# Kernel optimization log

Hardware: AMD Instinct MI355X
Metric: run time of the kernel (lower is better)

The kernel has to match this reference:

```python
import jax, jax.numpy as jnp
import numpy as np

B, N, D = 4, 2048, 512      # batch, seq, dim_in
DK = DV = 512               # dim_k == dim_v (required by fc input width)
NH = 8
HK = DK // NH               # per-head dk == dv == 64
SCALE = 1.0 / np.sqrt(HK)
LN_EPS = 1e-5


def setup_inputs() -> dict:
    key = jax.random.key(0)
    ks = jax.random.split(key, 8)
    s = 0.02
    return {
        "x": jax.random.normal(ks[0], (B, N, D), dtype=jnp.float32),
        "Wq": jax.random.normal(ks[1], (D, DK), dtype=jnp.float32) * s,
        "Wk": jax.random.normal(ks[2], (D, DK), dtype=jnp.float32) * s,
        "Wv": jax.random.normal(ks[3], (D, DV), dtype=jnp.float32) * s,
        "Wf": jax.random.normal(ks[4], (2 * DK, D), dtype=jnp.float32) * s,
        "bf": jnp.zeros((D,), dtype=jnp.float32),
        "gamma": jnp.ones((D,), dtype=jnp.float32),
        "beta": jnp.zeros((D,), dtype=jnp.float32),
    }


def reference(x, Wq, Wk, Wv, Wf, bf, gamma, beta):
    b, n, _ = x.shape
    # projections -> [b, nh, n, hk]; q_c/q_f etc. are identical in the source,
    # so compute once.
    def proj(W):
        return jnp.einsum('bnd,dk->bnk', x, W).reshape(b, n, NH, -1).transpose(0, 2, 1, 3)
    q, k, v = proj(Wq), proj(Wk), proj(Wv)

    # conventional branch: softmax over n x n scores
    dist_c = jax.nn.softmax(jnp.einsum('bhqd,bhkd->bhqk', q, k) * SCALE, axis=-1)
    att_c = jnp.einsum('bhqk,bhkd->bhqd', dist_c, v)          # [b,nh,n,hk]
    att_c = att_c.transpose(0, 2, 1, 3).reshape(b, n, DV)

    # feature branch: softmax over dk x dk scores (linear-complexity variant)
    dist_f = jax.nn.softmax(jnp.einsum('bhnk,bhnq->bhkq', k, q) * SCALE, axis=-1)
    att_f = jnp.einsum('bhnd,bhdq->bhnq', v, dist_f)           # [b,nh,n,hk]
    att_f = att_f.transpose(0, 2, 1, 3).reshape(b, n, DV)

    att = jnp.concatenate([att_c, att_f], axis=2)              # [b,n,2*dk]
    out = jax.nn.relu(att @ Wf + bf)                           # dropout=eval (identity)
    out = out + x
    mu = jnp.mean(out, axis=-1, keepdims=True)
    var = jnp.var(out, axis=-1, keepdims=True)
    out = (out - mu) * jax.lax.rsqrt(var + LN_EPS) * gamma + beta
    return out
```

## Files before the change

### kernel.cpp

```cpp
#include <hip/hip_runtime.h>
#include <math.h>
#include <stdint.h>

#define B_   4
#define N_   2048
#define D_   512
#define DK_  512
#define NH_  8
#define HK_  64
#define LN_EPS_ 1e-5f
#define QS_  0.18033688011112042f

typedef unsigned short u16;
typedef __attribute__((ext_vector_type(8))) short short8;
typedef __attribute__((ext_vector_type(4))) float f32x4;
typedef __attribute__((ext_vector_type(8))) unsigned short u16x8;

__device__ __forceinline__ u16 f2bf(float x) {
    uint32_t u = __builtin_bit_cast(uint32_t, x);
    return (u16)((u + 0x7fffu + ((u >> 16) & 1u)) >> 16);
}
__device__ __forceinline__ u16 f2bf_fast(float x) {
    return (u16)((__builtin_bit_cast(uint32_t, x) + 0x8000u) >> 16);
}
__device__ __forceinline__ float b2f(u16 v) {
    return __builtin_bit_cast(float, (uint32_t)v << 16);
}
__device__ __forceinline__ uint32_t cvtpk_bf16(float lo, float hi) {
    uint32_t r;
    asm("v_cvt_pk_bf16_f32 %0, %1, %2" : "=v"(r) : "v"(lo), "v"(hi));
    return r;
}
__device__ __forceinline__ float exp2f_fast(float x) {
    return __builtin_amdgcn_exp2f(x);
}

__device__ __forceinline__ void gload16(const void* g, void* l) {
    __builtin_amdgcn_global_load_lds(
        reinterpret_cast<const __attribute__((address_space(1))) void*>(
            reinterpret_cast<uintptr_t>(g)),
        reinterpret_cast<__attribute__((address_space(3))) void*>(
            static_cast<uint32_t>(reinterpret_cast<uintptr_t>(l))),
        16, 0, 0);
}

__global__ __launch_bounds__(256) void prep_kernel(
    const float* __restrict__ x, const float* __restrict__ Wq,
    const float* __restrict__ Wk, const float* __restrict__ Wv,
    const float* __restrict__ Wf, u16* __restrict__ xb,
    u16* __restrict__ wqkvT, u16* __restrict__ wfT)
{
    __shared__ float t[32][33];
    const int bid = blockIdx.x, tid = threadIdx.x;
    if (bid < 2048) {
        const int i = (bid * 256 + tid) * 8;
        const float4 a = *reinterpret_cast<const float4*>(&x[i]);
        const float4 b = *reinterpret_cast<const float4*>(&x[i + 4]);
        u16x8 o;
        o[0] = f2bf(a.x); o[1] = f2bf(a.y); o[2] = f2bf(a.z); o[3] = f2bf(a.w);
        o[4] = f2bf(b.x); o[5] = f2bf(b.y); o[6] = f2bf(b.z); o[7] = f2bf(b.w);
        *reinterpret_cast<u16x8*>(&xb[i]) = o;
        return;
    }
    const float* W;
    u16* dst;
    int K, Nc, nt, kt;
    if (bid < 2816) {
        const int z = (bid - 2048) >> 8, rem = (bid - 2048) & 255;
        W = z == 0 ? Wq : (z == 1 ? Wk : Wv);
        dst = wqkvT + (size_t)z * 512 * 512;
        K = 512; Nc = 512;
        nt = (rem & 15) * 32; kt = (rem >> 4) * 32;
    } else {
        const int rem = bid - 2816;
        W = Wf; dst = wfT; K = 1024; Nc = 512;
        nt = (rem & 15) * 32; kt = (rem >> 4) * 32;
    }
    {
        const int r = tid >> 3, c0 = (tid & 7) * 4;
        const float4 v = *reinterpret_cast<const float4*>(
            &W[(size_t)(kt + r) * Nc + nt + c0]);
        t[r][c0] = v.x; t[r][c0 + 1] = v.y; t[r][c0 + 2] = v.z; t[r][c0 + 3] = v.w;
    }
    __syncthreads();
    {
        const int nidx = tid >> 3, kc = (tid & 7) * 4;
        u16 o[4];
        #pragma unroll
        for (int j = 0; j < 4; ++j) o[j] = f2bf(t[kc + j][nidx]);
        *reinterpret_cast<ushort4*>(&dst[(size_t)(nt + nidx) * K + kt + kc]) =
            make_ushort4(o[0], o[1], o[2], o[3]);
    }
}

template<int BM, int BN, int MODE>
__global__ __launch_bounds__(256) void gemm_bf16(
    const u16* __restrict__ A, const u16* __restrict__ Bt,
    u16* __restrict__ qb, u16* __restrict__ kb,
    u16* __restrict__ vb, u16* __restrict__ vt, int M, int Nc, int K,
    const float* __restrict__ bias, const float* __restrict__ resid)
{
    constexpr int MI = BM / 32, NI = BN / 32;
    constexpr int AL = BM / 32, BL = BN / 32;
    __shared__ u16 As[BM * 64];
    __shared__ u16 Bs[BN * 64];
    const int tid = threadIdx.x;
    const int lane = tid & 63, wave = tid >> 6;
    const int wm = wave >> 1, wn = wave & 1;
    const int l15 = lane & 15, lg = lane >> 4;

    const int nwg = gridDim.x;
    const int bid = ((int)blockIdx.x & 7) * (nwg >> 3) + ((int)blockIdx.x >> 3);
    const int ntiles = Nc / BN;
    const int nt = (bid % ntiles) * BN;
    const int mt = (bid / ntiles) * BM;

    f32x4 acc[MI][NI] = {};

    for (int kt = 0; kt < K; kt += 64) {
        __syncthreads();
        #pragma unroll
        for (int i = 0; i < AL; ++i) {
            const int ob = (wave * AL + i) * 1024;
            const int o = ob + lane * 16;
            const int row = o >> 7;
            const int inner = (o & 127) ^ ((row & 7) << 4);
            gload16((const char*)A + ((size_t)(mt + row) * K + kt) * 2 + inner,
                    (char*)As + ob);
        }
        #pragma unroll
        for (int i = 0; i < BL; ++i) {
            const int ob = (wave * BL + i) * 1024;
            const int o = ob + lane * 16;
            const int row = o >> 7;
            const int inner = (o & 127) ^ ((row & 7) << 4);
            gload16((const char*)Bt + ((size_t)(nt + row) * K + kt) * 2 + inner,
                    (char*)Bs + ob);
        }
        __syncthreads();
        #pragma unroll
        for (int ks = 0; ks < 2; ++ks) {
            const int kb2 = ks * 32 + lg * 8;
            short8 af[MI], bfr[NI];
            #pragma unroll
            for (int mi = 0; mi < MI; ++mi) {
                const int r = wm * (BM / 2) + mi * 16 + l15;
                af[mi] = *reinterpret_cast<const short8*>(
                    &As[r * 64 + (kb2 ^ ((r & 7) << 3))]);
            }
            #pragma unroll
            for (int ni = 0; ni < NI; ++ni) {
                const int r = wn * (BN / 2) + ni * 16 + l15;
                bfr[ni] = *reinterpret_cast<const short8*>(
                    &Bs[r * 64 + (kb2 ^ ((r & 7) << 3))]);
            }
            #pragma unroll
            for (int mi = 0; mi < MI; ++mi)
                #pragma unroll
                for (int ni = 0; ni < NI; ++ni)
                    acc[mi][ni] = __builtin_amdgcn_mfma_f32_16x16x32_bf16(
                        af[mi], bfr[ni], acc[mi][ni], 0, 0, 0);
        }
    }

    #pragma unroll
    for (int mi = 0; mi < MI; ++mi) {
        #pragma unroll
        for (int ni = 0; ni < NI; ++ni) {
            const int col = nt + wn * (BN / 2) + ni * 16 + l15;
            const int row0 = mt + wm * (BM / 2) + mi * 16 + lg * 4;
            if (MODE == 1) {
                if (col < 512) {
                    #pragma unroll
                    for (int jj = 0; jj < 4; ++jj)
                        qb[(size_t)(row0 + jj) * 512 + col] =
                            f2bf(acc[mi][ni][jj] * QS_);
                } else if (col < 1024) {
                    #pragma unroll
                    for (int jj = 0; jj < 4; ++jj)
                        kb[(size_t)(row0 + jj) * 512 + col - 512] =
                            f2bf(acc[mi][ni][jj]);
                } else {
                    const int dfull = col - 1024;
                    const int hh = dfull >> 6, dd = dfull & 63;
                    const int bb = row0 >> 11, nn = row0 & 2047;
                    u16 o4[4];
                    #pragma unroll
                    for (int jj = 0; jj < 4; ++jj) {
                        o4[jj] = f2bf(acc[mi][ni][jj]);
                        vb[(size_t)(row0 + jj) * 512 + dfull] = o4[jj];
                    }
                    *reinterpret_cast<ushort4*>(
                        &vt[(((size_t)(bb * NH_ + hh)) * HK_ + dd) * N_ + nn]) =
                        make_ushort4(o4[0], o4[1], o4[2], o4[3]);
                }
            } else {
                #pragma unroll
                for (int jj = 0; jj < 4; ++jj) {
                    const size_t row = (size_t)(row0 + jj);
                    float v = acc[mi][ni][jj];
                    v += bias[col];
                    v = fmaxf(v, 0.0f);
                    v += resid[row * Nc + col];
                    qb[row * Nc + col] = f2bf(v);
                }
            }
        }
    }
}

__global__ __launch_bounds__(256) void flash_featS_kernel(
    const u16* __restrict__ Qb, const u16* __restrict__ Kb,
    const u16* __restrict__ Vt, u16* __restrict__ att,
    float* __restrict__ partials)
{
    __shared__ u16 sh[24576];
    const int tid = threadIdx.x;
    const int lane = tid & 63, wave = tid >> 6;
    const int l15 = lane & 15, lg = lane >> 4;

    if ((int)blockIdx.x >= 512) {
        u16* KsT = sh;
        u16* QsT = sh + 4096;
        const int fid = (int)blockIdx.x - 512;
        const int ns = fid & 7, h = (fid >> 3) & 7, b = fid >> 6;
        const size_t hbase = (size_t)b * N_ * DK_ + (size_t)h * HK_;

        f32x4 acc[4] = {};
        for (int c = 0; c < 4; ++c) {
            const int n0 = ns * 256 + c * 64;
            __syncthreads();
            #pragma unroll
            for (int it = 0; it < 2; ++it) {
                const int idx = tid + it * 256;
                const int n = idx >> 3, d0 = (idx & 7) * 8;
                const u16x8 kv = *reinterpret_cast<const u16x8*>(
                    &Kb[hbase + (size_t)(n0 + n) * DK_ + d0]);
                const u16x8 qv = *reinterpret_cast<const u16x8*>(
                    &Qb[hbase + (size_t)(n0 + n) * DK_ + d0]);
                #pragma unroll
                for (int j = 0; j < 8; ++j) {
                    const int r = d0 + j;
                    const int cidx = n ^ ((r & 7) << 3);
                    KsT[r * 64 + cidx] = kv[j];
                    QsT[r * 64 + cidx] = qv[j];
                }
            }
            __syncthreads();
            #pragma unroll
            for (int ks = 0; ks < 2; ++ks) {
                const int kb2 = ks * 32 + lg * 8;
                const int ar = wave * 16 + l15;
                const short8 aK = *reinterpret_cast<const short8*>(
                    &KsT[ar * 64 + (kb2 ^ ((ar & 7) << 3))]);
                #pragma unroll
                for (int ni = 0; ni < 4; ++ni) {
                    const int br = ni * 16 + l15;
                    const short8 bQ = *reinterpret_cast<const short8*>(
                        &QsT[br * 64 + (kb2 ^ ((br & 7) << 3))]);
                    acc[ni] = __builtin_amdgcn_mfma_f32_16x16x32_bf16(
                        aK, bQ, acc[ni], 0, 0, 0);
                }
            }
        }
        const int bh = b * NH_ + h;
        #pragma unroll
        for (int ni = 0; ni < 4; ++ni)
            #pragma unroll
            for (int jj = 0; jj < 4; ++jj) {
                const int row = wave * 16 + lg * 4 + jj;
                partials[(((size_t)ns * 32 + bh) * 64 + row) * 64 + ni * 16 + l15] =
                    acc[ni][jj];
            }
        return;
    }

    u16* kb0 = sh;
    u16* kb1 = sh + 4096;
    u16* vb0 = sh + 8192;
    u16* vb1 = sh + 12288;
    u16* Ps  = sh + 16384;
    const int lbid = (((int)blockIdx.x & 7) << 6) + ((int)blockIdx.x >> 3);
    const int qt = lbid & 15, h = (lbid >> 4) & 7, b = lbid >> 7;

    short8 aq[2][2];
    #pragma unroll
    for (int qs = 0; qs < 2; ++qs) {
        const int qrow = qt * 128 + qs * 64 + wave * 16 + l15;
        const u16* qp = Qb + ((size_t)(b * N_ + qrow)) * DK_ + h * HK_ + lg * 8;
        aq[qs][0] = *reinterpret_cast<const short8*>(qp);
        aq[qs][1] = *reinterpret_cast<const short8*>(qp + 32);
    }
    short8 ones;
    #pragma unroll
    for (int i = 0; i < 8; ++i) ones[i] = (short)0x3F80;

    const u16* Kbase = Kb + (size_t)b * N_ * DK_ + (size_t)h * HK_;
    const u16* Vbase = Vt + ((size_t)(b * NH_ + h)) * HK_ * N_;
    unsigned long long* Ps64 = reinterpret_cast<unsigned long long*>(Ps);

    f32x4 o[2][5] = {};
    float m_[2] = {-1e30f, -1e30f};
    f32x4 SA[2][4], SB[2][4];

    const int ob0 = wave * 1024, oo0 = ob0 + lane * 16;
    const int row0s = oo0 >> 7;
    const int in0 = (oo0 & 127) ^ ((row0s & 7) << 4);

#define STAGE_K(ktile, KBUF) do {                                              \
    gload16((const char*)Kbase +                                               \
                ((size_t)((ktile) * 64 + row0s) * DK_) * 2 + in0,              \
            (char*)(KBUF) + ob0);                                              \
    gload16((const char*)Kbase +                                               \
                ((size_t)((ktile) * 64 + 32 + row0s) * DK_) * 2 + in0,         \
            (char*)(KBUF) + 4096 + ob0);                                       \
} while (0)

#define STAGE_V(ktile, VBUF) do {                                              \
    gload16((const char*)Vbase +                                               \
                ((size_t)row0s * N_ + (ktile) * 64) * 2 + in0,                 \
            (char*)(VBUF) + ob0);                                              \
    gload16((const char*)Vbase +                                               \
                ((size_t)(32 + row0s) * N_ + (ktile) * 64) * 2 + in0,          \
            (char*)(VBUF) + 4096 + ob0);                                       \
} while (0)

#define QK_STEP(S, KBUF) do {                                                  \
    _Pragma("unroll")                                                          \
    for (int qs = 0; qs < 2; ++qs)                                             \
        _Pragma("unroll")                                                      \
        for (int t = 0; t < 4; ++t)                                            \
            S[qs][t] = (f32x4){0.0f, 0.0f, 0.0f, 0.0f};                        \
    __builtin_amdgcn_s_setprio(1);                                             \
    _Pragma("unroll")                                                          \
    for (int ks = 0; ks < 2; ++ks) {                                           \
        const int kb2 = ks * 32 + lg * 8;                                      \
        _Pragma("unroll")                                                      \
        for (int t = 0; t < 4; ++t) {                                          \
            const int r = t * 16 + l15;                                        \
            const short8 bk = *reinterpret_cast<const short8*>(                \
                &(KBUF)[r * 64 + (kb2 ^ ((r & 7) << 3))]);                     \
            S[0][t] = __builtin_amdgcn_mfma_f32_16x16x32_bf16(                 \
                bk, aq[0][ks], S[0][t], 0, 0, 0);                              \
            S[1][t] = __builtin_amdgcn_mfma_f32_16x16x32_bf16(                 \
                bk, aq[1][ks], S[1][t], 0, 0, 0);                              \
        }                                                                      \
    }                                                                          \
    __builtin_amdgcn_s_setprio(0);                                             \
} while (0)

#define SMPV_STEP(S, VBUF) do {                                                \
    float rmax[2], cm;                                                         \
    _Pragma("unroll")                                                          \
    for (int qs = 0; qs < 2; ++qs) {                                           \
        float a0 = fmaxf(fmaxf(S[qs][0][0], S[qs][0][1]),                      \
                         fmaxf(S[qs][0][2], S[qs][0][3]));                     \
        float a1 = fmaxf(fmaxf(S[qs][1][0], S[qs][1][1]),                      \
                         fmaxf(S[qs][1][2], S[qs][1][3]));                     \
        float a2 = fmaxf(fmaxf(S[qs][2][0], S[qs][2][1]),                      \
                         fmaxf(S[qs][2][2], S[qs][2][3]));                     \
        float a3 = fmaxf(fmaxf(S[qs][3][0], S[qs][3][1]),                      \
                         fmaxf(S[qs][3][2], S[qs][3][3]));                     \
        rmax[qs] = fmaxf(fmaxf(a0, a1), fmaxf(a2, a3));                        \
    }                                                                          \
    cm = fmaxf(rmax[0] - m_[0], rmax[1] - m_[1]);                              \
    if (__any(cm > 8.0f)) {                                                    \
        _Pragma("unroll")                                                      \
        for (int qs = 0; qs < 2; ++qs) {                                       \
            float rm = rmax[qs];                                               \
            rm = fmaxf(rm, __shfl_xor(rm, 16));                                \
            rm = fmaxf(rm, __shfl_xor(rm, 32));                                \
            const float newm = fmaxf(m_[qs], rm);                              \
            const float fac = exp2f_fast(m_[qs] - newm);                       \
            m_[qs] = newm;                                                     \
            float facq[4];                                                     \
            _Pragma("unroll")                                                  \
            for (int jj = 0; jj < 4; ++jj)                                     \
                facq[jj] = __shfl(fac, lg * 4 + jj);                           \
            _Pragma("unroll")                                                  \
            for (int t = 0; t < 5; ++t)                                        \
                _Pragma("unroll")                                              \
                for (int jj = 0; jj < 4; ++jj)                                 \
                    o[qs][t][jj] *= facq[jj];                                  \
        }                                                                      \
    }                                                                          \
    _Pragma("unroll")                                                          \
    for (int qs = 0; qs < 2; ++qs) {                                           \
        const int prow = qs * 64 + wave * 16 + l15;                            \
        const int pb64 = prow * 16;                                            \
        const int sw1 = (prow & 7) << 1;                                       \
        _Pragma("unroll")                                                      \
        for (int t = 0; t < 4; ++t) {                                          \
            const float p0 = exp2f_fast(S[qs][t][0] - m_[qs]);                 \
            const float p1 = exp2f_fast(S[qs][t][1] - m_[qs]);                 \
            const float p2 = exp2f_fast(S[qs][t][2] - m_[qs]);                 \
            const float p3 = exp2f_fast(S[qs][t][3] - m_[qs]);                 \
            const uint32_t lo = cvtpk_bf16(p0, p1);                            \
            const uint32_t hi = cvtpk_bf16(p2, p3);                            \
            Ps64[pb64 + ((t * 4 + lg) ^ sw1)] =                                \
                (unsigned long long)lo | ((unsigned long long)hi << 32);       \
        }                                                                      \
    }                                                                          \
    __builtin_amdgcn_s_setprio(1);                                             \
    _Pragma("unroll")                                                          \
    for (int ks = 0; ks < 2; ++ks) {                                           \
        const int kb2 = ks * 32 + lg * 8;                                      \
        const int pr0 = wave * 16 + l15;                                       \
        const int pr1 = 64 + pr0;                                              \
        const short8 ap0 = *reinterpret_cast<const short8*>(                   \
            &Ps[pr0 * 64 + (kb2 ^ ((pr0 & 7) << 3))]);                         \
        const short8 ap1 = *reinterpret_cast<const short8*>(                   \
            &Ps[pr1 * 64 + (kb2 ^ ((pr1 & 7) << 3))]);                         \
        _Pragma("unroll")                                                      \
        for (int t = 0; t < 4; ++t) {                                          \
            const int dr = t * 16 + l15;                                       \
            const short8 bv = *reinterpret_cast<const short8*>(                \
                &(VBUF)[dr * 64 + (kb2 ^ ((dr & 7) << 3))]);                   \
            o[0][t] = __builtin_amdgcn_mfma_f32_16x16x32_bf16(                 \
                ap0, bv, o[0][t], 0, 0, 0);                                    \
            o[1][t] = __builtin_amdgcn_mfma_f32_16x16x32_bf16(                 \
                ap1, bv, o[1][t], 0, 0, 0);                                    \
        }                                                                      \
        o[0][4] = __builtin_amdgcn_mfma_f32_16x16x32_bf16(                     \
            ap0, ones, o[0][4], 0, 0, 0);                                      \
        o[1][4] = __builtin_amdgcn_mfma_f32_16x16x32_bf16(                     \
            ap1, ones, o[1][4], 0, 0, 0);                                      \
    }                                                                          \
    __builtin_amdgcn_s_setprio(0);                                             \
} while (0)

    STAGE_K(0, kb0);
    STAGE_K(1, kb1);
    STAGE_V(0, vb0);
    __syncthreads();
    QK_STEP(SA, kb0);

    #pragma unroll 1
    for (int t2 = 0; t2 < 30; t2 += 2) {
        __syncthreads();
        STAGE_K(t2 + 2, kb0);
        STAGE_V(t2 + 1, vb1);
        QK_STEP(SB, kb1);
        SMPV_STEP(SA, vb0);
        __syncthreads();
        STAGE_K(t2 + 3, kb1);
        STAGE_V(t2 + 2, vb0);
        QK_STEP(SA, kb0);
        SMPV_STEP(SB, vb1);
    }
    __syncthreads();
    STAGE_V(31, vb1);
    QK_STEP(SB, kb1);
    SMPV_STEP(SA, vb0);
    __syncthreads();
    SMPV_STEP(SB, vb1);

#undef STAGE_K
#undef STAGE_V
#undef QK_STEP
#undef SMPV_STEP

    #pragma unroll
    for (int qs = 0; qs < 2; ++qs)
        #pragma unroll
        for (int jj = 0; jj < 4; ++jj) {
            const float inv = 1.0f / o[qs][4][jj];
            const size_t row = (size_t)b * N_ + qt * 128 + qs * 64 + wave * 16 + lg * 4 + jj;
            #pragma unroll
            for (int t = 0; t < 4; ++t)
                att[row * (2 * DK_) + h * HK_ + t * 16 + l15] =
                    f2bf_fast(o[qs][t][jj] * inv);
        }
}

__global__ __launch_bounds__(256) void featSM_kernel(
    const float* __restrict__ partials, u16* __restrict__ distfT)
{
    const int bh = blockIdx.x, tid = threadIdx.x;
    const int r = tid >> 2, qq = tid & 3;
    float v[16];
    #pragma unroll
    for (int j = 0; j < 16; ++j) v[j] = 0.0f;
    for (int s = 0; s < 8; ++s) {
        const float4* pp = reinterpret_cast<const float4*>(
            &partials[(((size_t)s * 32 + bh) * 64 + r) * 64 + qq * 16]);
        #pragma unroll
        for (int j4 = 0; j4 < 4; ++j4) {
            const float4 a = pp[j4];
            v[j4 * 4 + 0] += a.x; v[j4 * 4 + 1] += a.y;
            v[j4 * 4 + 2] += a.z; v[j4 * 4 + 3] += a.w;
        }
    }
    float m = v[0];
    #pragma unroll
    for (int j = 1; j < 16; ++j) m = fmaxf(m, v[j]);
    m = fmaxf(m, __shfl_xor(m, 1));
    m = fmaxf(m, __shfl_xor(m, 2));
    float sum = 0.0f;
    #pragma unroll
    for (int j = 0; j < 16; ++j) { v[j] = exp2f_fast(v[j] - m); sum += v[j]; }
    sum += __shfl_xor(sum, 1);
    sum += __shfl_xor(sum, 2);
    const float inv = 1.0f / sum;
    #pragma unroll
    for (int j = 0; j < 16; ++j)
        distfT[(size_t)bh * 4096 + (qq * 16 + j) * 64 + r] = f2bf_fast(v[j] * inv);
}

__global__ __launch_bounds__(256) void featAV_mfma(
    const u16* __restrict__ V, const u16* __restrict__ distfT,
    u16* __restrict__ att)
{
    __shared__ u16 Bs[64 * 64];
    __shared__ u16 As[64 * 64];
    const int tid = threadIdx.x;
    const int lane = tid & 63, wave = tid >> 6;
    const int l15 = lane & 15, lg = lane >> 4;
    const int ns = blockIdx.x, h = blockIdx.y, b = blockIdx.z;
    const int bh = b * NH_ + h;

    #pragma unroll
    for (int it = 0; it < 2; ++it) {
        const int idx = tid + it * 256;
        const int r = idx >> 3, c0 = (idx & 7) * 8;
        const u16x8 dv = *reinterpret_cast<const u16x8*>(
            &distfT[(size_t)bh * 4096 + r * 64 + c0]);
        *reinterpret_cast<u16x8*>(&Bs[r * 64 + (c0 ^ ((r & 7) << 3))]) = dv;
    }

    for (int c = 0; c < 4; ++c) {
        const int n0 = ns * 256 + c * 64;
        __syncthreads();
        #pragma unroll
        for (int i = 0; i < 2; ++i) {
            const int ob = (wave * 2 + i) * 1024;
            const int o_ = ob + lane * 16;
            const int row = o_ >> 7;
            const int inner = (o_ & 127) ^ ((row & 7) << 4);
            gload16((const char*)V + ((size_t)(b * N_ + n0 + row) * DK_ + h * HK_) * 2 + inner,
                    (char*)As + ob);
        }
        __syncthreads();
        f32x4 acc[4] = {};
        #pragma unroll
        for (int ks = 0; ks < 2; ++ks) {
            const int kb2 = ks * 32 + lg * 8;
            const int ar = wave * 16 + l15;
            const short8 av = *reinterpret_cast<const short8*>(
                &As[ar * 64 + (kb2 ^ ((ar & 7) << 3))]);
            #pragma unroll
            for (int ni = 0; ni < 4; ++ni) {
                const int br = ni * 16 + l15;
                const short8 bd = *reinterpret_cast<const short8*>(
                    &Bs[br * 64 + (kb2 ^ ((br & 7) << 3))]);
                acc[ni] = __builtin_amdgcn_mfma_f32_16x16x32_bf16(av, bd, acc[ni], 0, 0, 0);
            }
        }
        #pragma unroll
        for (int ni = 0; ni < 4; ++ni)
            #pragma unroll
            for (int jj = 0; jj < 4; ++jj)
                att[((size_t)b * N_ + n0 + wave * 16 + lg * 4 + jj) * (2 * DK_)
                    + 512 + h * HK_ + ni * 16 + l15] = f2bf_fast(acc[ni][jj]);
    }
}

__global__ __launch_bounds__(256) void ln_kernel(
    const u16* __restrict__ fc, const float* __restrict__ gamma,
    const float* __restrict__ beta, float* __restrict__ out)
{
    const int row = blockIdx.x * 4 + (threadIdx.x >> 6);
    const int lane = threadIdx.x & 63;
    const int c = lane * 8;
    const u16x8 v = *reinterpret_cast<const u16x8*>(&fc[(size_t)row * D_ + c]);
    float f[8];
    float s = 0.0f, sq = 0.0f;
    #pragma unroll
    for (int j = 0; j < 8; ++j) {
        f[j] = b2f(v[j]);
        s += f[j];
        sq = fmaf(f[j], f[j], sq);
    }
    #pragma unroll
    for (int off = 32; off >= 1; off >>= 1) {
        s  += __shfl_xor(s, off);
        sq += __shfl_xor(sq, off);
    }
    const float mu = s * (1.0f / D_);
    const float var = sq * (1.0f / D_) - mu * mu;
    const float rstd = rsqrtf(var + LN_EPS_);
    const float4 g0 = *reinterpret_cast<const float4*>(&gamma[c]);
    const float4 g1 = *reinterpret_cast<const float4*>(&gamma[c + 4]);
    const float4 b0 = *reinterpret_cast<const float4*>(&beta[c]);
    const float4 b1 = *reinterpret_cast<const float4*>(&beta[c + 4]);
    const float gg[8] = {g0.x, g0.y, g0.z, g0.w, g1.x, g1.y, g1.z, g1.w};
    const float bb[8] = {b0.x, b0.y, b0.z, b0.w, b1.x, b1.y, b1.z, b1.w};
    float4 o0, o1;
    o0.x = (f[0] - mu) * rstd * gg[0] + bb[0];
    o0.y = (f[1] - mu) * rstd * gg[1] + bb[1];
    o0.z = (f[2] - mu) * rstd * gg[2] + bb[2];
    o0.w = (f[3] - mu) * rstd * gg[3] + bb[3];
    o1.x = (f[4] - mu) * rstd * gg[4] + bb[4];
    o1.y = (f[5] - mu) * rstd * gg[5] + bb[5];
    o1.z = (f[6] - mu) * rstd * gg[6] + bb[6];
    o1.w = (f[7] - mu) * rstd * gg[7] + bb[7];
    *reinterpret_cast<float4*>(&out[(size_t)row * D_ + c]) = o0;
    *reinterpret_cast<float4*>(&out[(size_t)row * D_ + c + 4]) = o1;
}

extern "C" void kernel_launch(void* const* d_in, const int* in_sizes, int n_in,
                              void* d_out, int out_size, void* d_ws, size_t ws_size,
                              hipStream_t stream)
{
    (void)in_sizes; (void)n_in; (void)out_size; (void)ws_size;
    const float* x     = (const float*)d_in[0];
    const float* Wq    = (const float*)d_in[1];
    const float* Wk    = (const float*)d_in[2];
    const float* Wv    = (const float*)d_in[3];
    const float* Wf    = (const float*)d_in[4];
    const float* bf    = (const float*)d_in[5];
    const float* gamma = (const float*)d_in[6];
    const float* beta  = (const float*)d_in[7];
    float* out = (float*)d_out;

    char* w = (char*)d_ws;
    const size_t SZE = (size_t)B_ * N_ * DK_;
    u16* xb     = (u16*)w;   w += SZE * 2;
    u16* wqkvT  = (u16*)w;   w += (size_t)1536 * 512 * 2;
    u16* wfT    = (u16*)w;   w += (size_t)512 * 1024 * 2;
    u16* qb     = (u16*)w;   w += SZE * 2;
    u16* kb     = (u16*)w;   w += SZE * 2;
    u16* vb     = (u16*)w;   w += SZE * 2;
    u16* vt     = (u16*)w;   w += SZE * 2;
    u16* attb   = (u16*)w;   w += SZE * 2 * 2;
    float* partials = (float*)w; w += (size_t)8 * 32 * 4096 * 4;
    u16* distfT = (u16*)w;   w += (size_t)32 * 4096 * 2;
    u16* fcout  = (u16*)w;

    const dim3 blk(256);
    const int M = B_ * N_;

    prep_kernel<<<dim3(3328), blk, 0, stream>>>(x, Wq, Wk, Wv, Wf, xb, wqkvT, wfT);

    gemm_bf16<128, 128, 1><<<dim3(768), blk, 0, stream>>>(
        xb, wqkvT, qb, kb, vb, vt, M, 1536, 512, nullptr, nullptr);

    flash_featS_kernel<<<dim3(768), blk, 0, stream>>>(qb, kb, vt, attb, partials);

    featSM_kernel<<<dim3(32), blk, 0, stream>>>(partials, distfT);
    featAV_mfma<<<dim3(8, NH_, B_), blk, 0, stream>>>(vb, distfT, attb);

    gemm_bf16<64, 128, 2><<<dim3(512), blk, 0, stream>>>(
        attb, wfT, fcout, nullptr, nullptr, nullptr, M, D_, 2 * DK_, bf, x);

    ln_kernel<<<dim3(2048), blk, 0, stream>>>(fcout, gamma, beta, out);
}
```

Baseline: 126.2 us.

## Fuse feature-branch score, softmax and AV into flash kernel tail blocks

The feature-branch blocks inside the flash kernel now each own one (batch, head): they accumulate the full 64x64 K^T Q scores over all 2048 rows, apply the softmax in registers, stage the bf16 distribution in shared memory, and then compute V·dist for every row. This removes the separate partial-score buffer, the softmax kernel and the AV kernel along with their launches and global round trips. In exchange, only 32 feature blocks remain instead of 256, each running a long serial loop over 32 chunks twice, so the feature branch may become the tail of the flash launch.

```diff
diff --git a/kernel.cpp b/kernel.cpp
--- a/kernel.cpp
+++ b/kernel.cpp
@@ -209,10 +209,10 @@
     }
 }
 
-__global__ __launch_bounds__(256) void flash_featS_kernel(
+__global__ __launch_bounds__(256) void flash_feat_kernel(
     const u16* __restrict__ Qb, const u16* __restrict__ Kb,
-    const u16* __restrict__ Vt, u16* __restrict__ att,
-    float* __restrict__ partials)
+    const u16* __restrict__ Vt, const u16* __restrict__ Vb,
+    u16* __restrict__ att)
 {
     __shared__ u16 sh[24576];
     const int tid = threadIdx.x;
@@ -222,13 +222,15 @@
     if ((int)blockIdx.x >= 512) {
         u16* KsT = sh;
         u16* QsT = sh + 4096;
+        u16* BsD = sh + 8192;
+        u16* AsV = sh;
         const int fid = (int)blockIdx.x - 512;
-        const int ns = fid & 7, h = (fid >> 3) & 7, b = fid >> 6;
+        const int h = fid & 7, b = fid >> 3;
         const size_t hbase = (size_t)b * N_ * DK_ + (size_t)h * HK_;
 
         f32x4 acc[4] = {};
-        for (int c = 0; c < 4; ++c) {
-            const int n0 = ns * 256 + c * 64;
+        for (int c = 0; c < 32; ++c) {
+            const int n0 = c * 64;
             __syncthreads();
             #pragma unroll
             for (int it = 0; it < 2; ++it) {
@@ -263,15 +265,80 @@
                 }
             }
         }
-        const int bh = b * NH_ + h;
+
+        float dv[4][4];
         #pragma unroll
-        for (int ni = 0; ni < 4; ++ni)
-            #pragma unroll
-            for (int jj = 0; jj < 4; ++jj) {
-                const int row = wave * 16 + lg * 4 + jj;
-                partials[(((size_t)ns * 32 + bh) * 64 + row) * 64 + ni * 16 + l15] =
-                    acc[ni][jj];
-            }
+        for (int jj = 0; jj < 4; ++jj) {
+            float tm = fmaxf(fmaxf(acc[0][jj], acc[1][jj]),
+                             fmaxf(acc[2][jj], acc[3][jj]));
+            tm = fmaxf(tm, __shfl_xor(tm, 1));
+            tm = fmaxf(tm, __shfl_xor(tm, 2));
+            tm = fmaxf(tm, __shfl_xor(tm, 4));
+            tm = fmaxf(tm, __shfl_xor(tm, 8));
+            float rs = 0.0f;
+            #pragma unroll
+            for (int ni = 0; ni < 4; ++ni) {
+                dv[ni][jj] = exp2f_fast(acc[ni][jj] - tm);
+                rs += dv[ni][jj];
+            }
+            rs += __shfl_xor(rs, 1);
+            rs += __shfl_xor(rs, 2);
+            rs += __shfl_xor(rs, 4);
+            rs += __shfl_xor(rs, 8);
+            const float inv = 1.0f / rs;
+            #pragma unroll
+            for (int ni = 0; ni < 4; ++ni) dv[ni][jj] *= inv;
+        }
+        {
+            unsigned long long* Bs64 = reinterpret_cast<unsigned long long*>(BsD);
+            const int kd0 = wave * 16 + lg * 4;
+            #pragma unroll
+            for (int ni = 0; ni < 4; ++ni) {
+                const int q = ni * 16 + l15;
+                const uint32_t lo = cvtpk_bf16(dv[ni][0], dv[ni][1]);
+                const uint32_t hi = cvtpk_bf16(dv[ni][2], dv[ni][3]);
+                Bs64[q * 16 + ((kd0 ^ ((q & 7) << 3)) >> 2)] =
+                    (unsigned long long)lo | ((unsigned long long)hi << 32);
+            }
+        }
+
+        for (int c = 0; c < 32; ++c) {
+            const int n0 = c * 64;
+            __syncthreads();
+            #pragma unroll
+            for (int i = 0; i < 2; ++i) {
+                const int ob = (wave * 2 + i) * 1024;
+                const int o_ = ob + lane * 16;
+                const int row = o_ >> 7;
+                const int inner = (o_ & 127) ^ ((row & 7) << 4);
+                gload16((const char*)Vb +
+                            ((size_t)(b * N_ + n0 + row) * DK_ + h * HK_) * 2 + inner,
+                        (char*)AsV + ob);
+            }
+            __syncthreads();
+            f32x4 oacc[4] = {};
+            #pragma unroll
+            for (int ks = 0; ks < 2; ++ks) {
+                const int kb2 = ks * 32 + lg * 8;
+                const int ar = wave * 16 + l15;
+                const short8 av = *reinterpret_cast<const short8*>(
+                    &AsV[ar * 64 + (kb2 ^ ((ar & 7) << 3))]);
+                #pragma unroll
+                for (int ni = 0; ni < 4; ++ni) {
+                    const int br = ni * 16 + l15;
+                    const short8 bd = *reinterpret_cast<const short8*>(
+                        &BsD[br * 64 + (kb2 ^ ((br & 7) << 3))]);
+                    oacc[ni] = __builtin_amdgcn_mfma_f32_16x16x32_bf16(
+                        av, bd, oacc[ni], 0, 0, 0);
+                }
+            }
+            #pragma unroll
+            for (int ni = 0; ni < 4; ++ni)
+                #pragma unroll
+                for (int jj = 0; jj < 4; ++jj)
+                    att[((size_t)b * N_ + n0 + wave * 16 + lg * 4 + jj) * (2 * DK_)
+                        + 512 + h * HK_ + ni * 16 + l15] = f2bf_fast(oacc[ni][jj]);
+        }
         return;
     }
 
@@ -473,98 +540,6 @@
         }
 }
 
-__global__ __launch_bounds__(256) void featSM_kernel(
-    const float* __restrict__ partials, u16* __restrict__ distfT)
-{
-    const int bh = blockIdx.x, tid = threadIdx.x;
-    const int r = tid >> 2, qq = tid & 3;
-    float v[16];
-    #pragma unroll
-    for (int j = 0; j < 16; ++j) v[j] = 0.0f;
-    for (int s = 0; s < 8; ++s) {
-        const float4* pp = reinterpret_cast<const float4*>(
-            &partials[(((size_t)s * 32 + bh) * 64 + r) * 64 + qq * 16]);
-        #pragma unroll
-        for (int j4 = 0; j4 < 4; ++j4) {
-            const float4 a = pp[j4];
-            v[j4 * 4 + 0] += a.x; v[j4 * 4 + 1] += a.y;
-            v[j4 * 4 + 2] += a.z; v[j4 * 4 + 3] += a.w;
-        }
-    }
-    float m = v[0];
-    #pragma unroll
-    for (int j = 1; j < 16; ++j) m = fmaxf(m, v[j]);
-    m = fmaxf(m, __shfl_xor(m, 1));
-    m = fmaxf(m, __shfl_xor(m, 2));
-    float sum = 0.0f;
-    #pragma unroll
-    for (int j = 0; j < 16; ++j) { v[j] = exp2f_fast(v[j] - m); sum += v[j]; }
-    sum += __shfl_xor(sum, 1);
-    sum += __shfl_xor(sum, 2);
-    const float inv = 1.0f / sum;
-    #pragma unroll
-    for (int j = 0; j < 16; ++j)
-        distfT[(size_t)bh * 4096 + (qq * 16 + j) * 64 + r] = f2bf_fast(v[j] * inv);
-}
-
-__global__ __launch_bounds__(256) void featAV_mfma(
-    const u16* __restrict__ V, const u16* __restrict__ distfT,
-    u16* __restrict__ att)
-{
-    __shared__ u16 Bs[64 * 64];
-    __shared__ u16 As[64 * 64];
-    const int tid = threadIdx.x;
-    const int lane = tid & 63, wave = tid >> 6;
-    const int l15 = lane & 15, lg = lane >> 4;
-    const int ns = blockIdx.x, h = blockIdx.y, b = blockIdx.z;
-    const int bh = b * NH_ + h;
-
-    #pragma unroll
-    for (int it = 0; it < 2; ++it) {
-        const int idx = tid + it * 256;
-        const int r = idx >> 3, c0 = (idx & 7) * 8;
-        const u16x8 dv = *reinterpret_cast<const u16x8*>(
-            &distfT[(size_t)bh * 4096 + r * 64 + c0]);
-        *reinterpret_cast<u16x8*>(&Bs[r * 64 + (c0 ^ ((r & 7) << 3))]) = dv;
-    }
-
-    for (int c = 0; c < 4; ++c) {
-        const int n0 = ns * 256 + c * 64;
-        __syncthreads();
-        #pragma unroll
-        for (int i = 0; i < 2; ++i) {
-            const int ob = (wave * 2 + i) * 1024;
-            const int o_ = ob + lane * 16;
-            const int row = o_ >> 7;
-            const int inner = (o_ & 127) ^ ((row & 7) << 4);
-            gload16((const char*)V + ((size_t)(b * N_ + n0 + row) * DK_ + h * HK_) * 2 + inner,
-                    (char*)As + ob);
-        }
-        __syncthreads();
-        f32x4 acc[4] = {};
-        #pragma unroll
-        for (int ks = 0; ks < 2; ++ks) {
-            const int kb2 = ks * 32 + lg * 8;
-            const int ar = wave * 16 + l15;
-            const short8 av = *reinterpret_cast<const short8*>(
-                &As[ar * 64 + (kb2 ^ ((ar & 7) << 3))]);
-            #pragma unroll
-            for (int ni = 0; ni < 4; ++ni) {
-                const int br = ni * 16 + l15;
-                const short8 bd = *reinterpret_cast<const short8*>(
-                    &Bs[br * 64 + (kb2 ^ ((br & 7) << 3))]);
-                acc[ni] = __builtin_amdgcn_mfma_f32_16x16x32_bf16(av, bd, acc[ni], 0, 0, 0);
-            }
-        }
-        #pragma unroll
-        for (int ni = 0; ni < 4; ++ni)
-            #pragma unroll
-            for (int jj = 0; jj < 4; ++jj)
-                att[((size_t)b * N_ + n0 + wave * 16 + lg * 4 + jj) * (2 * DK_)
-                    + 512 + h * HK_ + ni * 16 + l15] = f2bf_fast(acc[ni][jj]);
-    }
-}
-
 __global__ __launch_bounds__(256) void ln_kernel(
     const u16* __restrict__ fc, const float* __restrict__ gamma,
     const float* __restrict__ beta, float* __restrict__ out)
@@ -633,8 +608,6 @@
     u16* vb     = (u16*)w;   w += SZE * 2;
     u16* vt     = (u16*)w;   w += SZE * 2;
     u16* attb   = (u16*)w;   w += SZE * 2 * 2;
-    float* partials = (float*)w; w += (size_t)8 * 32 * 4096 * 4;
-    u16* distfT = (u16*)w;   w += (size_t)32 * 4096 * 2;
     u16* fcout  = (u16*)w;
 
     const dim3 blk(256);
@@ -645,10 +618,7 @@
     gemm_bf16<128, 128, 1><<<dim3(768), blk, 0, stream>>>(
         xb, wqkvT, qb, kb, vb, vt, M, 1536, 512, nullptr, nullptr);
 
-    flash_featS_kernel<<<dim3(768), blk, 0, stream>>>(qb, kb, vt, attb, partials);
-
-    featSM_kernel<<<dim3(32), blk, 0, stream>>>(partials, distfT);
-    featAV_mfma<<<dim3(8, NH_, B_), blk, 0, stream>>>(vb, distfT, attb);
+    flash_feat_kernel<<<dim3(544), blk, 0, stream>>>(qb, kb, vt, vb, attb);
 
     gemm_bf16<64, 128, 2><<<dim3(512), blk, 0, stream>>>(
         attb, wfT, fcout, nullptr, nullptr, nullptr, M, D_, 2 * DK_, bf, x);
```

Result: slower. 174.6 us (+38.3%).

## Widen featSM/featAV grids and add double-buffered FC GEMM with swizzled block order

Applied to the files above, without the earlier changes.

The feature-softmax kernel now launches 128 blocks instead of 32, with 16 threads per row and wider shuffle reductions. featAV now uses one 64-row chunk per block, giving 4x more blocks and no serial loop. The output projection moves to a dedicated GEMM that double-buffers LDS and remaps block indices to improve L2 reuse. The aim is more parallelism and better load/compute overlap in small tail kernels, at the cost of reloading distfT in every featAV block and of more code.

```diff
diff --git a/kernel.cpp b/kernel.cpp
--- a/kernel.cpp
+++ b/kernel.cpp
@@ -204,6 +204,103 @@
                     v += resid[row * Nc + col];
                     qb[row * Nc + col] = f2bf(v);
                 }
+            }
+        }
+    }
+}
+
+__global__ __launch_bounds__(256) void gemm_fc_kernel(
+    const u16* __restrict__ A, const u16* __restrict__ Bt,
+    u16* __restrict__ C, const float* __restrict__ bias,
+    const float* __restrict__ resid)
+{
+    __shared__ u16 As0[64 * 64], As1[64 * 64];
+    __shared__ u16 Bs0[128 * 64], Bs1[128 * 64];
+    const int tid = threadIdx.x;
+    const int lane = tid & 63, wave = tid >> 6;
+    const int wm = wave >> 1, wn = wave & 1;
+    const int l15 = lane & 15, lg = lane >> 4;
+    const int bid = ((int)blockIdx.x & 7) * 64 + ((int)blockIdx.x >> 3);
+    const int nt = (bid & 3) * 128;
+    const int mt = (bid >> 2) * 64;
+
+    f32x4 acc[2][4] = {};
+
+#define FC_STAGE(kt, AS, BS) do {                                              \
+    _Pragma("unroll")                                                          \
+    for (int i_ = 0; i_ < 2; ++i_) {                                           \
+        const int ob_ = (wave * 2 + i_) * 1024;                                \
+        const int o_ = ob_ + lane * 16;                                        \
+        const int row_ = o_ >> 7;                                              \
+        const int inner_ = (o_ & 127) ^ ((row_ & 7) << 4);                     \
+        gload16((const char*)A + ((size_t)(mt + row_) * 1024 + (kt) * 64) * 2  \
+                    + inner_, (char*)(AS) + ob_);                              \
+    }                                                                          \
+    _Pragma("unroll")                                                          \
+    for (int i_ = 0; i_ < 4; ++i_) {                                           \
+        const int ob_ = (wave * 4 + i_) * 1024;                                \
+        const int o_ = ob_ + lane * 16;                                        \
+        const int row_ = o_ >> 7;                                              \
+        const int inner_ = (o_ & 127) ^ ((row_ & 7) << 4);                     \
+        gload16((const char*)Bt + ((size_t)(nt + row_) * 1024 + (kt) * 64) * 2 \
+                    + inner_, (char*)(BS) + ob_);                              \
+    }                                                                          \
+} while (0)
+
+#define FC_COMP(AS, BS) do {                                                   \
+    _Pragma("unroll")                                                          \
+    for (int ks = 0; ks < 2; ++ks) {                                           \
+        const int kb2 = ks * 32 + lg * 8;                                      \
+        short8 af[2], bfr[4];                                                  \
+        _Pragma("unroll")                                                      \
+        for (int mi = 0; mi < 2; ++mi) {                                       \
+            const int r = wm * 32 + mi * 16 + l15;                             \
+            af[mi] = *reinterpret_cast<const short8*>(                         \
+                &(AS)[r * 64 + (kb2 ^ ((r & 7) << 3))]);                       \
+        }                                                                      \
+        _Pragma("unroll")                                                      \
+        for (int ni = 0; ni < 4; ++ni) {                                       \
+            const int r = wn * 64 + ni * 16 + l15;                             \
+            bfr[ni] = *reinterpret_cast<const short8*>(                        \
+                &(BS)[r * 64 + (kb2 ^ ((r & 7) << 3))]);                       \
+        }                                                                      \
+        _Pragma("unroll")                                                      \
+        for (int mi = 0; mi < 2; ++mi)                                         \
+            _Pragma("unroll")                                                  \
+            for (int ni = 0; ni < 4; ++ni)                                     \
+                acc[mi][ni] = __builtin_amdgcn_mfma_f32_16x16x32_bf16(         \
+                    af[mi], bfr[ni], acc[mi][ni], 0, 0, 0);                    \
+    }                                                                          \
+} while (0)
+
+    FC_STAGE(0, As0, Bs0);
+    __syncthreads();
+    #pragma unroll 1
+    for (int kt = 0; kt < 16; kt += 2) {
+        FC_STAGE(kt + 1, As1, Bs1);
+        FC_COMP(As0, Bs0);
+        __syncthreads();
+        if (kt + 2 < 16) FC_STAGE(kt + 2, As0, Bs0);
+        FC_COMP(As1, Bs1);
+        __syncthreads();
+    }
+#undef FC_STAGE
+#undef FC_COMP
+
+    #pragma unroll
+    for (int mi = 0; mi < 2; ++mi) {
+        #pragma unroll
+        for (int ni = 0; ni < 4; ++ni) {
+            const int col = nt + wn * 64 + ni * 16 + l15;
+            const int row0 = mt + wm * 32 + mi * 16 + lg * 4;
+            #pragma unroll
+            for (int jj = 0; jj < 4; ++jj) {
+                const size_t row = (size_t)(row0 + jj);
+                float v = acc[mi][ni][jj];
+                v += bias[col];
+                v = fmaxf(v, 0.0f);
+                v += resid[row * 512 + col];
+                C[row * 512 + col] = f2bf(v);
             }
         }
     }
@@ -476,35 +573,31 @@
 __global__ __launch_bounds__(256) void featSM_kernel(
     const float* __restrict__ partials, u16* __restrict__ distfT)
 {
-    const int bh = blockIdx.x, tid = threadIdx.x;
-    const int r = tid >> 2, qq = tid & 3;
-    float v[16];
-    #pragma unroll
-    for (int j = 0; j < 16; ++j) v[j] = 0.0f;
+    const int bh = blockIdx.x, rg = blockIdx.y, tid = threadIdx.x;
+    const int r = rg * 16 + (tid >> 4);
+    const int tl = tid & 15;
+    float v[4] = {0.0f, 0.0f, 0.0f, 0.0f};
     for (int s = 0; s < 8; ++s) {
-        const float4* pp = reinterpret_cast<const float4*>(
-            &partials[(((size_t)s * 32 + bh) * 64 + r) * 64 + qq * 16]);
-        #pragma unroll
-        for (int j4 = 0; j4 < 4; ++j4) {
-            const float4 a = pp[j4];
-            v[j4 * 4 + 0] += a.x; v[j4 * 4 + 1] += a.y;
-            v[j4 * 4 + 2] += a.z; v[j4 * 4 + 3] += a.w;
-        }
-    }
-    float m = v[0];
-    #pragma unroll
-    for (int j = 1; j < 16; ++j) m = fmaxf(m, v[j]);
+        const float4 a = *reinterpret_cast<const float4*>(
+            &partials[(((size_t)s * 32 + bh) * 64 + r) * 64 + tl * 4]);
+        v[0] += a.x; v[1] += a.y; v[2] += a.z; v[3] += a.w;
+    }
+    float m = fmaxf(fmaxf(v[0], v[1]), fmaxf(v[2], v[3]));
     m = fmaxf(m, __shfl_xor(m, 1));
     m = fmaxf(m, __shfl_xor(m, 2));
+    m = fmaxf(m, __shfl_xor(m, 4));
+    m = fmaxf(m, __shfl_xor(m, 8));
     float sum = 0.0f;
     #pragma unroll
-    for (int j = 0; j < 16; ++j) { v[j] = exp2f_fast(v[j] - m); sum += v[j]; }
+    for (int j = 0; j < 4; ++j) { v[j] = exp2f_fast(v[j] - m); sum += v[j]; }
     sum += __shfl_xor(sum, 1);
     sum += __shfl_xor(sum, 2);
+    sum += __shfl_xor(sum, 4);
+    sum += __shfl_xor(sum, 8);
     const float inv = 1.0f / sum;
     #pragma unroll
-    for (int j = 0; j < 16; ++j)
-        distfT[(size_t)bh * 4096 + (qq * 16 + j) * 64 + r] = f2bf_fast(v[j] * inv);
+    for (int j = 0; j < 4; ++j)
+        distfT[(size_t)bh * 4096 + (tl * 4 + j) * 64 + r] = f2bf_fast(v[j] * inv);
 }
 
 __global__ __launch_bounds__(256) void featAV_mfma(
@@ -518,6 +611,7 @@
     const int l15 = lane & 15, lg = lane >> 4;
     const int ns = blockIdx.x, h = blockIdx.y, b = blockIdx.z;
     const int bh = b * NH_ + h;
+    const int n0 = ns * 64;
 
     #pragma unroll
     for (int it = 0; it < 2; ++it) {
@@ -527,42 +621,37 @@
             &distfT[(size_t)bh * 4096 + r * 64 + c0]);
         *reinterpret_cast<u16x8*>(&Bs[r * 64 + (c0 ^ ((r & 7) << 3))]) = dv;
     }
-
-    for (int c = 0; c < 4; ++c) {
-        const int n0 = ns * 256 + c * 64;
-        __syncthreads();
-        #pragma unroll
-        for (int i = 0; i < 2; ++i) {
-            const int ob = (wave * 2 + i) * 1024;
-            const int o_ = ob + lane * 16;
-            const int row = o_ >> 7;
-            const int inner = (o_ & 127) ^ ((row & 7) << 4);
-            gload16((const char*)V + ((size_t)(b * N_ + n0 + row) * DK_ + h * HK_) * 2 + inner,
-                    (char*)As + ob);
+    #pragma unroll
+    for (int i = 0; i < 2; ++i) {
+        const int ob = (wave * 2 + i) * 1024;
+        const int o_ = ob + lane * 16;
+        const int row = o_ >> 7;
+        const int inner = (o_ & 127) ^ ((row & 7) << 4);
+        gload16((const char*)V + ((size_t)(b * N_ + n0 + row) * DK_ + h * HK_) * 2 + inner,
+                (char*)As + ob);
+    }
+    __syncthreads();
+    f32x4 acc[4] = {};
+    #pragma unroll
+    for (int ks = 0; ks < 2; ++ks) {
+        const int kb2 = ks * 32 + lg * 8;
+        const int ar = wave * 16 + l15;
+        const short8 av = *reinterpret_cast<const short8*>(
+            &As[ar * 64 + (kb2 ^ ((ar & 7) << 3))]);
+        #pragma unroll
+        for (int ni = 0; ni < 4; ++ni) {
+            const int br = ni * 16 + l15;
+            const short8 bd = *reinterpret_cast<const short8*>(
+                &Bs[br * 64 + (kb2 ^ ((br & 7) << 3))]);
+            acc[ni] = __builtin_amdgcn_mfma_f32_16x16x32_bf16(av, bd, acc[ni], 0, 0, 0);
         }
-        __syncthreads();
-        f32x4 acc[4] = {};
-        #pragma unroll
-        for (int ks = 0; ks < 2; ++ks) {
-            const int kb2 = ks * 32 + lg * 8;
-            const int ar = wave * 16 + l15;
-            const short8 av = *reinterpret_cast<const short8*>(
-                &As[ar * 64 + (kb2 ^ ((ar & 7) << 3))]);
-            #pragma unroll
-            for (int ni = 0; ni < 4; ++ni) {
-                const int br = ni * 16 + l15;
-                const short8 bd = *reinterpret_cast<const short8*>(
-                    &Bs[br * 64 + (kb2 ^ ((br & 7) << 3))]);
-                acc[ni] = __builtin_amdgcn_mfma_f32_16x16x32_bf16(av, bd, acc[ni], 0, 0, 0);
-            }
-        }
-        #pragma unroll
-        for (int ni = 0; ni < 4; ++ni)
-            #pragma unroll
-            for (int jj = 0; jj < 4; ++jj)
-                att[((size_t)b * N_ + n0 + wave * 16 + lg * 4 + jj) * (2 * DK_)
-                    + 512 + h * HK_ + ni * 16 + l15] = f2bf_fast(acc[ni][jj]);
-    }
+    }
+    #pragma unroll
+    for (int ni = 0; ni < 4; ++ni)
+        #pragma unroll
+        for (int jj = 0; jj < 4; ++jj)
+            att[((size_t)b * N_ + n0 + wave * 16 + lg * 4 + jj) * (2 * DK_)
+                + 512 + h * HK_ + ni * 16 + l15] = f2bf_fast(acc[ni][jj]);
 }
 
 __global__ __launch_bounds__(256) void ln_kernel(
@@ -647,11 +736,10 @@
 
     flash_featS_kernel<<<dim3(768), blk, 0, stream>>>(qb, kb, vt, attb, partials);
 
-    featSM_kernel<<<dim3(32), blk, 0, stream>>>(partials, distfT);
-    featAV_mfma<<<dim3(8, NH_, B_), blk, 0, stream>>>(vb, distfT, attb);
-
-    gemm_bf16<64, 128, 2><<<dim3(512), blk, 0, stream>>>(
-        attb, wfT, fcout, nullptr, nullptr, nullptr, M, D_, 2 * DK_, bf, x);
+    featSM_kernel<<<dim3(32, 4), blk, 0, stream>>>(partials, distfT);
+    featAV_mfma<<<dim3(32, NH_, B_), blk, 0, stream>>>(vb, distfT, attb);
+
+    gemm_fc_kernel<<<dim3(512), blk, 0, stream>>>(attb, wfT, fcout, bf, x);
 
     ln_kernel<<<dim3(2048), blk, 0, stream>>>(fcout, gamma, beta, out);
 }
```

Result: faster. 120.6 us (-4.5%).
